# Kernel tuning notes

Measured on AMD Instinct MI355X. Metric: run time of the kernel, lower is better.

## Reference

```python
import jax, jax.numpy as jnp
import numpy as np

H = 8          # n_heads
LORA_SCALE = 1.0


def _lora(x, down, up):
    # nn.Linear convention: y = x @ W.T ; down:[r,in], up:[out,r]
    return (x @ down.T) @ up.T


def setup_inputs() -> dict:
    key = jax.random.key(0)
    ks = jax.random.split(key, 16)
    B, S, D, R = 4, 2048, 640, 4
    std = 1.0 / np.sqrt(D)
    inp = {
        "hidden_states": jax.random.normal(ks[0], (B, S, D), jnp.float32),
        "wq": jax.random.normal(ks[1], (D, D), jnp.float32) * std,
        "wk": jax.random.normal(ks[2], (D, D), jnp.float32) * std,
        "wv": jax.random.normal(ks[3], (D, D), jnp.float32) * std,
        "wo": jax.random.normal(ks[4], (D, D), jnp.float32) * std,
        "bo": jax.random.normal(ks[5], (D,), jnp.float32) * 0.02,
        "q_down": jax.random.normal(ks[6], (R, D), jnp.float32) * (1.0 / R),
        "q_up": jax.random.normal(ks[7], (D, R), jnp.float32) * 0.02,
        "k_down": jax.random.normal(ks[8], (R, D), jnp.float32) * (1.0 / R),
        "k_up": jax.random.normal(ks[9], (D, R), jnp.float32) * 0.02,
        "v_down": jax.random.normal(ks[10], (R, D), jnp.float32) * (1.0 / R),
        "v_up": jax.random.normal(ks[11], (D, R), jnp.float32) * 0.02,
        "o_down": jax.random.normal(ks[12], (R, D), jnp.float32) * (1.0 / R),
        "o_up": jax.random.normal(ks[13], (D, R), jnp.float32) * 0.02,
    }
    return inp


def reference(hidden_states, wq, wk, wv, wo, bo,
              q_down, q_up, k_down, k_up, v_down, v_up, o_down, o_up):
    B, S, D = hidden_states.shape
    hd = D // H
    sm_scale = 1.0 / np.sqrt(hd)

    x = hidden_states  # self-attention: encoder_hidden_states = hidden_states
    q = x @ wq.T + LORA_SCALE * _lora(x, q_down, q_up)
    k = x @ wk.T + LORA_SCALE * _lora(x, k_down, k_up)
    v = x @ wv.T + LORA_SCALE * _lora(x, v_down, v_up)

    # head_to_batch_dim: [B,S,D] -> [B,H,S,hd]
    q = q.reshape(B, S, H, hd).transpose(0, 2, 1, 3)
    k = k.reshape(B, S, H, hd).transpose(0, 2, 1, 3)
    v = v.reshape(B, S, H, hd).transpose(0, 2, 1, 3)

    # get_attention_scores: baddbmm(beta=0, alpha=1/sqrt(hd)) + softmax
    scores = jnp.einsum("bhqd,bhkd->bhqk", q, k) * sm_scale
    probs = jax.nn.softmax(scores, axis=-1)
    attn_out = jnp.einsum("bhqk,bhkd->bhqd", probs, v)

    # batch_to_head_dim: [B,H,S,hd] -> [B,S,D]
    attn_out = attn_out.transpose(0, 2, 1, 3).reshape(B, S, D)

    # out projection (with bias) + LoRA on the pre-projection hidden states
    out = attn_out @ wo.T + bo + LORA_SCALE * _lora(attn_out, o_down, o_up)
    # to_out[1] is dropout -> identity at eval
    return out
```

## Files before the change

### kernel.cpp

```cpp
#include <hip/hip_runtime.h>

typedef unsigned short u16;
typedef unsigned int u32;
typedef unsigned long long u64;

typedef __bf16 bf16x8 __attribute__((ext_vector_type(8)));
typedef float f32x4 __attribute__((ext_vector_type(4)));
typedef float f32x16 __attribute__((ext_vector_type(16)));

__device__ __forceinline__ float b2f(u16 u) {
    union { u32 i; float f; } c; c.i = ((u32)u) << 16; return c.f;
}
__device__ __forceinline__ u16 f2b(float f) {
    union { float f; u32 i; } c; c.f = f;
    u32 r = c.i + 0x7fffu + ((c.i >> 16) & 1u);
    return (u16)(r >> 16);
}
__device__ __forceinline__ u32 pack2(float a, float b) {
    return (u32)f2b(a) | ((u32)f2b(b) << 16);
}
__device__ __forceinline__ u32 cvt_pk_bf16(float a, float b) {
    u32 r;
    asm("v_cvt_pk_bf16_f32 %0, %1, %2" : "=v"(r) : "v"(a), "v"(b));
    return r;
}
__device__ __forceinline__ float fexp2(float x) {
    float r;
    asm("v_exp_f32 %0, %1" : "=v"(r) : "v"(x));
    return r;
}

__device__ __forceinline__ f32x4 mfma16(bf16x8 a, bf16x8 b, f32x4 c) {
    return __builtin_amdgcn_mfma_f32_16x16x32_bf16(a, b, c, 0, 0, 0);
}
__device__ __forceinline__ f32x16 mfma32(bf16x8 a, bf16x8 b, f32x16 c) {
    return __builtin_amdgcn_mfma_f32_32x32x16_bf16(a, b, c, 0, 0, 0);
}

__device__ __forceinline__ void lds_cp16(const u16* gsrc, u16* ldst) {
    __builtin_amdgcn_global_load_lds(
        (const __attribute__((address_space(1))) u32*)gsrc,
        (__attribute__((address_space(3))) u32*)ldst, 16, 0, 0);
}

struct ConvJobs {
    const float* s[4];
    const float* up[4];
    const float* dn[4];
    u16* d[4];
};

__global__ __launch_bounds__(256) void prep(ConvJobs J,
                                            const float* __restrict__ x,
                                            u16* __restrict__ xb,
                                            u16* __restrict__ vt, int do_pad) {
    int bx = blockIdx.x;
    if (bx < 1600) {
        int j = bx / 400;
        int i = (bx - j * 400) * 256 + threadIdx.x;
        int n = i / 160;
        int k4 = (i - n * 160) * 4;
        float4 w = ((const float4*)J.s[j])[i];
        float4 u = *(const float4*)(J.up[j] + n * 4);
        const float* dnp = J.dn[j];
        float4 d0 = *(const float4*)(dnp + k4);
        float4 d1 = *(const float4*)(dnp + 640 + k4);
        float4 d2 = *(const float4*)(dnp + 1280 + k4);
        float4 d3 = *(const float4*)(dnp + 1920 + k4);
        ushort4 o;
        o.x = f2b(w.x + u.x * d0.x + u.y * d1.x + u.z * d2.x + u.w * d3.x);
        o.y = f2b(w.y + u.x * d0.y + u.y * d1.y + u.z * d2.y + u.w * d3.y);
        o.z = f2b(w.z + u.x * d0.z + u.y * d1.z + u.z * d2.z + u.w * d3.z);
        o.w = f2b(w.w + u.x * d0.w + u.y * d1.w + u.z * d2.w + u.w * d3.w);
        ((ushort4*)J.d[j])[i] = o;
    } else if (bx < 2880) {
        int base = (bx - 1600) * 1024 + threadIdx.x;
#pragma unroll
        for (int it = 0; it < 4; ++it) {
            int i = base + it * 256;
            float4 v = ((const float4*)x)[i];
            ushort4 o;
            o.x = f2b(v.x); o.y = f2b(v.y); o.z = f2b(v.z); o.w = f2b(v.w);
            ((ushort4*)xb)[i] = o;
        }
    } else if (do_pad) {
        int idx = (bx - 2880) * 256 + threadIdx.x;
        int q = idx * 4;
        int bh = q >> 15;
        int rem = q & 32767;
        int row = rem >> 11, col = rem & 2047;
        u16 val = (row == 0) ? (u16)0x3F80 : (u16)0;
        ushort4 o = make_ushort4(val, val, val, val);
        *(ushort4*)(vt + ((size_t)bh * 96 + 80 + row) * 2048 + col) = o;
    }
}

struct QkvPtrs {
    const u16* W[3];
    void* out[3];
    float scale[3];
    int mode[3];
};

__global__ __launch_bounds__(256) void gemm_bt(const u16* __restrict__ A, QkvPtrs P,
                                               const float* __restrict__ bias) {
    int z = blockIdx.z;
    const u16* W = P.W[z];
    const float scl = P.scale[z];
    const int md = P.mode[z];
    int m0 = blockIdx.x * 128, n0 = blockIdx.y * 128;
    int tid = threadIdx.x, lane = tid & 63, wid = tid >> 6;
    int g = lane >> 4, l15 = lane & 15;
    __shared__ __align__(16) u16 smem[24576];
    u16* As_ = smem;
    u16* Bs_ = smem + 12288;
    f32x4 acc[4][4] = {};
    int wm = (wid & 1) * 64, wn = (wid >> 1) * 64;

    int r0 = tid >> 2, cb = (tid & 3) * 8;
    const u16* pA = A + (size_t)(m0 + r0) * 640 + cb;
    const u16* pB = W + (size_t)(n0 + r0) * 640 + cb;

    auto stage = [&](int buf, int k0) {
        u16* da = As_ + buf * 4096 + tid * 8;
        u16* db = Bs_ + buf * 4096 + tid * 8;
        lds_cp16(pA + k0, da);
        lds_cp16(pA + 40960 + k0, da + 2048);
        lds_cp16(pB + k0, db);
        lds_cp16(pB + 40960 + k0, db + 2048);
    };
    auto compute = [&](int cur) {
        const u16* as = As_ + cur * 4096;
        const u16* bs = Bs_ + cur * 4096;
        bf16x8 af[4], bfv[4];
#pragma unroll
        for (int q4 = 0; q4 < 4; ++q4) {
            af[q4]  = *(const bf16x8*)(as + (wm + q4 * 16 + l15) * 32 + g * 8);
            bfv[q4] = *(const bf16x8*)(bs + (wn + q4 * 16 + l15) * 32 + g * 8);
        }
#pragma unroll
        for (int i = 0; i < 4; ++i)
#pragma unroll
            for (int j = 0; j < 4; ++j)
                acc[i][j] = mfma16(af[i], bfv[j], acc[i][j]);
    };

    stage(0, 0);
    stage(1, 32);
    int cur = 0;
    for (int t = 0; t < 19; ++t) {
        asm volatile("s_waitcnt vmcnt(4)" ::: "memory");
        __builtin_amdgcn_s_barrier();
        asm volatile("" ::: "memory");
        if (t < 18) stage((cur == 0) ? 2 : cur - 1, (t + 2) * 32);
        compute(cur);
        cur = (cur == 2) ? 0 : cur + 1;
    }
    asm volatile("s_waitcnt vmcnt(0)" ::: "memory");
    __builtin_amdgcn_s_barrier();
    asm volatile("" ::: "memory");
    compute(cur);

    float bv[4];
#pragma unroll
    for (int j = 0; j < 4; ++j) {
        int n = n0 + wn + j * 16 + l15;
        bv[j] = (md == 1) ? bias[n] : 0.f;
    }

    if (md == 2) {
        __syncthreads();
        u16* Tl = smem;
#pragma unroll
        for (int i = 0; i < 4; ++i) {
#pragma unroll
            for (int j = 0; j < 4; ++j) {
                uint2 pk;
                pk.x = pack2(acc[i][j][0], acc[i][j][1]);
                pk.y = pack2(acc[i][j][2], acc[i][j][3]);
                *(uint2*)(Tl + (wn + j * 16 + l15) * 136 + wm + i * 16 + g * 4) = pk;
            }
        }
        __syncthreads();
        int bb2 = m0 >> 11;
        int sl0 = m0 & 2047;
        u16* outb_ = (u16*)P.out[z];
#pragma unroll
        for (int it = 0; it < 16; ++it) {
            int qq = it * 256 + tid;
            int row = qq >> 5;
            int pos = (qq & 31) * 4;
            int ss = (pos & ~12) | ((pos & 4) << 1) | ((pos & 8) >> 1);
            uint2 val = *(const uint2*)(Tl + row * 136 + ss);
            int n = n0 + row;
            int h = n / 80, d = n - h * 80;
            *(uint2*)(outb_ + (((size_t)bb2 * 8 + h) * 96 + d) * 2048 + sl0 + pos) = val;
        }
        return;
    }

    float* outf = (float*)P.out[z];
    u16* outb = (u16*)P.out[z];
#pragma unroll
    for (int i = 0; i < 4; ++i) {
#pragma unroll
        for (int r = 0; r < 4; ++r) {
            int m = m0 + wm + i * 16 + g * 4 + r;
#pragma unroll
            for (int j = 0; j < 4; ++j) {
                int n = n0 + wn + j * 16 + l15;
                float v = acc[i][j][r] + bv[j];
                if (md == 1) {
                    outf[(size_t)m * 640 + n] = v;
                } else {
                    int bb = m >> 11, s = m & 2047;
                    int h = n / 80, d = n - h * 80;
                    outb[(((size_t)bb * 8 + h) * 2048 + s) * 80 + d] = f2b(v * scl);
                }
            }
        }
    }
}

__global__ __launch_bounds__(256) void transpose_v(const u16* __restrict__ Vin,
                                                   u16* __restrict__ Vout) {
    __shared__ u32 lds32[64 * 41];
    int bh = blockIdx.y;
    int s0 = blockIdx.x * 64;
    int tid = threadIdx.x;
    const u16* in = Vin + (size_t)bh * 2048 * 80;
    u16* out = Vout + (size_t)bh * 96 * 2048;

    for (int t = tid; t < 640; t += 256) {
        int s = t / 10, c = t - s * 10;
        uint4 v = *(const uint4*)(in + (size_t)(s0 + s) * 80 + c * 8);
        u32* p = lds32 + s * 41 + c * 4;
        p[0] = v.x; p[1] = v.y; p[2] = v.z; p[3] = v.w;
    }
    __syncthreads();
    for (int t = tid; t < 640; t += 256) {
        int d = t >> 3, c8 = t & 7;
        int dp = d >> 1, hi = d & 1;
        u16 vals[8];
#pragma unroll
        for (int j = 0; j < 8; ++j) {
            u32 w = lds32[(c8 * 8 + j) * 41 + dp];
            vals[j] = hi ? (u16)(w >> 16) : (u16)(w & 0xffff);
        }
        u16* dst = out + (size_t)d * 2048 + s0 + (c8 >> 1) * 16 + (c8 & 1) * 4;
        *(uint2*)dst = *(const uint2*)(vals);
        *(uint2*)(dst + 8) = *(const uint2*)(vals + 4);
    }
    for (int t = tid; t < 1024; t += 256) {
        int r = t >> 6, c = t & 63;
        out[(size_t)(80 + r) * 2048 + s0 + c] = (r == 0) ? 0x3F80 : 0;
    }
}

__global__ __launch_bounds__(512) void flash_attn(const u16* __restrict__ Q,
                                                  const u16* __restrict__ K,
                                                  const u16* __restrict__ Vt_g,
                                                  u16* __restrict__ O) {
    int bh = blockIdx.y;
    int q0 = blockIdx.x * 256;
    int tid = threadIdx.x;
    int lane = tid & 63, wid = tid >> 6, l31 = lane & 31, h2 = lane >> 5;
    const size_t base = (size_t)bh * 2048 * 80;
    const size_t vbase = (size_t)bh * 96 * 2048;

    __shared__ __align__(16) u16 lds[2 * 5632 + 2 * 7200];
    u16* Ks0 = lds;
    u16* Vt0 = lds + 11264;

    bf16x8 qf[5];
    {
        int qrow = q0 + wid * 32 + l31;
#pragma unroll
        for (int ks = 0; ks < 5; ++ks)
            qf[ks] = *(const bf16x8*)(Q + base + (size_t)qrow * 80 + ks * 16 + h2 * 8);
    }

    f32x16 oa[3] = {};
    const float C2 = 17.312340490667562f;

    auto stage = [&](int buf, int kt) {
#pragma unroll
        for (int it = 0; it < 4; ++it) {
            int c = tid + it * 512;
            if (c < 704) {
                int row = c / 11, col = c - row * 11;
                lds_cp16(K + base + (size_t)(kt + row) * 80 + col * 8,
                         Ks0 + buf * 5632 + c * 8);
            } else if (c < 1600) {
                int t = c - 704;
                int row = t / 9, col = t - row * 9;
                lds_cp16(Vt_g + vbase + (size_t)row * 2048 + kt + col * 8,
                         Vt0 + buf * 7200 + t * 8);
            }
        }
    };

    stage(0, 0);
    __syncthreads();

    for (int i = 0; i < 32; ++i) {
        int cur = i & 1;
        if (i < 31) stage(cur ^ 1, (i + 1) * 64);

        const u16* ks = Ks0 + cur * 5632;
        const u16* vt = Vt0 + cur * 7200;

#pragma unroll
        for (int kk2 = 0; kk2 < 2; ++kk2) {
            f32x16 s = {};
            __builtin_amdgcn_s_setprio(1);
#pragma unroll
            for (int ks5 = 0; ks5 < 5; ++ks5) {
                bf16x8 kf = *(const bf16x8*)(ks + (kk2 * 32 + l31) * 88 + ks5 * 16 + h2 * 8);
                s = mfma32(kf, qf[ks5], s);
            }
            __builtin_amdgcn_s_setprio(0);
            u32 d[8];
#pragma unroll
            for (int j = 0; j < 8; ++j)
                d[j] = cvt_pk_bf16(fexp2(s[2 * j] - C2), fexp2(s[2 * j + 1] - C2));
            __builtin_amdgcn_s_setprio(1);
#pragma unroll
            for (int sl = 0; sl < 2; ++sl) {
                union { u32 w[4]; bf16x8 v; } pa;
                pa.w[0] = d[4 * sl + 0];
                pa.w[1] = d[4 * sl + 1];
                pa.w[2] = d[4 * sl + 2];
                pa.w[3] = d[4 * sl + 3];
#pragma unroll
                for (int nt = 0; nt < 3; ++nt) {
                    bf16x8 vf = *(const bf16x8*)(vt + (nt * 32 + l31) * 72 +
                                                 kk2 * 32 + sl * 16 + h2 * 8);
                    oa[nt] = mfma32(pa.v, vf, oa[nt]);
                }
            }
            __builtin_amdgcn_s_setprio(0);
        }
        __syncthreads();
    }

    int b = bh >> 3, h = bh & 7;
    float inv[16];
#pragma unroll
    for (int reg = 0; reg < 16; ++reg)
        inv[reg] = 1.f / __shfl(oa[2][reg], (lane & 32) + 16, 64);
#pragma unroll
    for (int nt = 0; nt < 3; ++nt) {
        int vd = nt * 32 + l31;
        if (vd < 80) {
#pragma unroll
            for (int reg = 0; reg < 16; ++reg) {
                int q = q0 + wid * 32 + (reg & 3) + 8 * (reg >> 2) + 4 * h2;
                O[((size_t)(b * 2048 + q)) * 640 + h * 80 + vd] = f2b(oa[nt][reg] * inv[reg]);
            }
        }
    }
}

extern "C" void kernel_launch(void* const* d_in, const int* in_sizes, int n_in,
                              void* d_out, int out_size, void* d_ws, size_t ws_size,
                              hipStream_t stream) {
    const float* x      = (const float*)d_in[0];
    const float* wq     = (const float*)d_in[1];
    const float* wk     = (const float*)d_in[2];
    const float* wv     = (const float*)d_in[3];
    const float* wo     = (const float*)d_in[4];
    const float* bo     = (const float*)d_in[5];
    const float* q_down = (const float*)d_in[6];
    const float* q_up   = (const float*)d_in[7];
    const float* k_down = (const float*)d_in[8];
    const float* k_up   = (const float*)d_in[9];
    const float* v_down = (const float*)d_in[10];
    const float* v_up   = (const float*)d_in[11];
    const float* o_down = (const float*)d_in[12];
    const float* o_up   = (const float*)d_in[13];

    char* ws = (char*)d_ws;
    u16* xb    = (u16*)(ws);
    u16* wbv   = (u16*)(ws + 10485760);
    u16* wbq   = (u16*)(ws + 11304960);
    u16* wbk   = (u16*)(ws + 12124160);
    u16* wbo   = (u16*)(ws + 12943360);
    u16* q_ws  = (u16*)(ws + 13762560);
    u16* k_ws  = (u16*)(ws + 24248320);
    u16* v_ws  = (u16*)(ws + 34734080);
    u16* attn  = (u16*)(ws + 45219840);

    const size_t vt_off = 56360960;
    const size_t vt_need = vt_off + 12582912 + 16384;
    const bool direct_vt = (ws_size >= vt_need);
    u16* vT_ws = direct_vt ? (u16*)(ws + vt_off)
                           : (u16*)(ws);

    ConvJobs cj;
    cj.s[0] = wq; cj.up[0] = q_up; cj.dn[0] = q_down; cj.d[0] = wbq;
    cj.s[1] = wk; cj.up[1] = k_up; cj.dn[1] = k_down; cj.d[1] = wbk;
    cj.s[2] = wv; cj.up[2] = v_up; cj.dn[2] = v_down; cj.d[2] = wbv;
    cj.s[3] = wo; cj.up[3] = o_up; cj.dn[3] = o_down; cj.d[3] = wbo;
    prep<<<3904, 256, 0, stream>>>(cj, x, xb, vT_ws, direct_vt ? 1 : 0);

    QkvPtrs pq;
    pq.W[0] = wbq; pq.W[1] = wbk; pq.W[2] = wbv;
    pq.out[0] = q_ws; pq.out[1] = k_ws;
    pq.out[2] = direct_vt ? (void*)vT_ws : (void*)v_ws;
    pq.scale[0] = 0.11180339887498949f * 1.4426950408889634f;
    pq.scale[1] = 1.0f;
    pq.scale[2] = 1.0f;
    pq.mode[0] = 0; pq.mode[1] = 0; pq.mode[2] = direct_vt ? 2 : 0;
    gemm_bt<<<dim3(64, 5, 3), 256, 0, stream>>>(xb, pq, bo);

    if (!direct_vt)
        transpose_v<<<dim3(32, 32), 256, 0, stream>>>(v_ws, vT_ws);

    flash_attn<<<dim3(8, 32), 512, 0, stream>>>(q_ws, k_ws, vT_ws, attn);

    QkvPtrs po;
    po.W[0] = wbo; po.W[1] = wbo; po.W[2] = wbo;
    po.out[0] = d_out; po.out[1] = d_out; po.out[2] = d_out;
    po.scale[0] = 1.0f; po.scale[1] = 1.0f; po.scale[2] = 1.0f;
    po.mode[0] = 1; po.mode[1] = 1; po.mode[2] = 1;
    gemm_bt<<<dim3(64, 5, 1), 256, 0, stream>>>(attn, po, bo);
}
```

Measured before the change: 193.8 us.

## Fuse prep, QKV GEMM, flash attention and out-proj into one persistent kernel

Replaces the chain of separate launches (weight/activation prep, QKV GEMM, flash attention, output projection) with a single 256-block persistent kernel whose phases are separated by atomic-counter grid barriers. The GEMM phases are rewritten for 512-thread blocks with a different per-wave tile, and the flash attention body is factored into a shared device function. The aim is to remove launch overhead and inter-kernel gaps. In exchange, GEMM tiles now run on a fixed 256-block grid with several tiles per block, and the spin barriers assume all 256 blocks are co-resident, which risks deadlock if they are not.

```diff
diff --git a/kernel.cpp b/kernel.cpp
--- a/kernel.cpp
+++ b/kernel.cpp
@@ -50,10 +50,323 @@
     u16* d[4];
 };
 
-__global__ __launch_bounds__(256) void prep(ConvJobs J,
-                                            const float* __restrict__ x,
-                                            u16* __restrict__ xb,
-                                            u16* __restrict__ vt, int do_pad) {
+__device__ __forceinline__ void gridbar(u32* cnt, int idx) {
+    __syncthreads();
+    __threadfence();
+    if (threadIdx.x == 0) {
+        atomicAdd(&cnt[idx], 1u);
+        while (atomicAdd(&cnt[idx], 0u) < 256u) __builtin_amdgcn_s_sleep(2);
+    }
+    __syncthreads();
+    __threadfence();
+}
+
+__device__ __forceinline__ void gemm_tile512(const u16* __restrict__ Ap,
+                                             const u16* __restrict__ W,
+                                             void* outp, float scl, int md,
+                                             const float* __restrict__ bias,
+                                             int m0, int n0, u16* smem) {
+    int tid = threadIdx.x, lane = tid & 63, wid = tid >> 6;
+    int g = lane >> 4, l15 = lane & 15;
+    u16* As_ = smem;
+    u16* Bs_ = smem + 12288;
+    f32x4 acc[4][2] = {};
+    int wm = (wid & 1) * 64, wn = (wid >> 1) * 32;
+
+    int r0 = tid >> 2, cb = (tid & 3) * 8;
+    const u16* pA = Ap + (size_t)(m0 + r0) * 640 + cb;
+    const u16* pB = W + (size_t)(n0 + r0) * 640 + cb;
+
+    __syncthreads();
+
+    auto stage = [&](int buf, int k0) {
+        lds_cp16(pA + k0, As_ + buf * 4096 + tid * 8);
+        lds_cp16(pB + k0, Bs_ + buf * 4096 + tid * 8);
+    };
+    auto compute = [&](int cur) {
+        const u16* as = As_ + cur * 4096;
+        const u16* bs = Bs_ + cur * 4096;
+        bf16x8 af[4], bfv[2];
+#pragma unroll
+        for (int i = 0; i < 4; ++i)
+            af[i] = *(const bf16x8*)(as + (wm + i * 16 + l15) * 32 + g * 8);
+#pragma unroll
+        for (int j = 0; j < 2; ++j)
+            bfv[j] = *(const bf16x8*)(bs + (wn + j * 16 + l15) * 32 + g * 8);
+#pragma unroll
+        for (int i = 0; i < 4; ++i)
+#pragma unroll
+            for (int j = 0; j < 2; ++j)
+                acc[i][j] = mfma16(af[i], bfv[j], acc[i][j]);
+    };
+
+    stage(0, 0);
+    stage(1, 32);
+    int cur = 0;
+    for (int t = 0; t < 19; ++t) {
+        asm volatile("s_waitcnt vmcnt(2)" ::: "memory");
+        __builtin_amdgcn_s_barrier();
+        asm volatile("" ::: "memory");
+        if (t < 18) stage((cur == 0) ? 2 : cur - 1, (t + 2) * 32);
+        compute(cur);
+        cur = (cur == 2) ? 0 : cur + 1;
+    }
+    asm volatile("s_waitcnt vmcnt(0)" ::: "memory");
+    __builtin_amdgcn_s_barrier();
+    asm volatile("" ::: "memory");
+    compute(cur);
+
+    if (md == 2) {
+        __syncthreads();
+        u16* Tl = smem;
+#pragma unroll
+        for (int i = 0; i < 4; ++i) {
+#pragma unroll
+            for (int j = 0; j < 2; ++j) {
+                uint2 pk;
+                pk.x = pack2(acc[i][j][0], acc[i][j][1]);
+                pk.y = pack2(acc[i][j][2], acc[i][j][3]);
+                *(uint2*)(Tl + (wn + j * 16 + l15) * 136 + wm + i * 16 + g * 4) = pk;
+            }
+        }
+        __syncthreads();
+        int bb2 = m0 >> 11;
+        int sl0 = m0 & 2047;
+        u16* outb_ = (u16*)outp;
+#pragma unroll
+        for (int it = 0; it < 8; ++it) {
+            int qq = it * 512 + tid;
+            int row = qq >> 5;
+            int pos = (qq & 31) * 4;
+            int ss = (pos & ~12) | ((pos & 4) << 1) | ((pos & 8) >> 1);
+            uint2 val = *(const uint2*)(Tl + row * 136 + ss);
+            int n = n0 + row;
+            int h = n / 80, d = n - h * 80;
+            *(uint2*)(outb_ + (((size_t)bb2 * 8 + h) * 96 + d) * 2048 + sl0 + pos) = val;
+        }
+        __syncthreads();
+        return;
+    }
+
+    float bv[2];
+#pragma unroll
+    for (int j = 0; j < 2; ++j)
+        bv[j] = (md == 1) ? bias[n0 + wn + j * 16 + l15] : 0.f;
+    float* outf = (float*)outp;
+    u16* outb = (u16*)outp;
+#pragma unroll
+    for (int i = 0; i < 4; ++i) {
+#pragma unroll
+        for (int r = 0; r < 4; ++r) {
+            int m = m0 + wm + i * 16 + g * 4 + r;
+#pragma unroll
+            for (int j = 0; j < 2; ++j) {
+                int n = n0 + wn + j * 16 + l15;
+                float v = acc[i][j][r] + bv[j];
+                if (md == 1) {
+                    outf[(size_t)m * 640 + n] = v;
+                } else {
+                    int bb = m >> 11, s = m & 2047;
+                    int h = n / 80, d = n - h * 80;
+                    outb[(((size_t)bb * 8 + h) * 2048 + s) * 80 + d] = f2b(v * scl);
+                }
+            }
+        }
+    }
+}
+
+__device__ __forceinline__ void flash512(int bid, const u16* __restrict__ Q,
+                                         const u16* __restrict__ K,
+                                         const u16* __restrict__ Vt_g,
+                                         u16* __restrict__ O, u16* lds) {
+    int q0 = (bid & 7) * 256;
+    int bh = bid >> 3;
+    int tid = threadIdx.x;
+    int lane = tid & 63, wid = tid >> 6, l31 = lane & 31, h2 = lane >> 5;
+    const size_t base = (size_t)bh * 2048 * 80;
+    const size_t vbase = (size_t)bh * 96 * 2048;
+
+    u16* Ks0 = lds;
+    u16* Vt0 = lds + 11264;
+
+    bf16x8 qf[5];
+    {
+        int qrow = q0 + wid * 32 + l31;
+#pragma unroll
+        for (int ks = 0; ks < 5; ++ks)
+            qf[ks] = *(const bf16x8*)(Q + base + (size_t)qrow * 80 + ks * 16 + h2 * 8);
+    }
+
+    f32x16 oa[3] = {};
+    const float C2 = 17.312340490667562f;
+
+    auto stage = [&](int buf, int kt) {
+#pragma unroll
+        for (int it = 0; it < 4; ++it) {
+            int c = tid + it * 512;
+            if (c < 704) {
+                int row = c / 11, col = c - row * 11;
+                lds_cp16(K + base + (size_t)(kt + row) * 80 + col * 8,
+                         Ks0 + buf * 5632 + c * 8);
+            } else if (c < 1600) {
+                int t = c - 704;
+                int row = t / 9, col = t - row * 9;
+                lds_cp16(Vt_g + vbase + (size_t)row * 2048 + kt + col * 8,
+                         Vt0 + buf * 7200 + t * 8);
+            }
+        }
+    };
+
+    stage(0, 0);
+    __syncthreads();
+
+    for (int i = 0; i < 32; ++i) {
+        int cur = i & 1;
+        if (i < 31) stage(cur ^ 1, (i + 1) * 64);
+
+        const u16* ks = Ks0 + cur * 5632;
+        const u16* vt = Vt0 + cur * 7200;
+
+#pragma unroll
+        for (int kk2 = 0; kk2 < 2; ++kk2) {
+            f32x16 s = {};
+            __builtin_amdgcn_s_setprio(1);
+#pragma unroll
+            for (int ks5 = 0; ks5 < 5; ++ks5) {
+                bf16x8 kf = *(const bf16x8*)(ks + (kk2 * 32 + l31) * 88 + ks5 * 16 + h2 * 8);
+                s = mfma32(kf, qf[ks5], s);
+            }
+            __builtin_amdgcn_s_setprio(0);
+            u32 d[8];
+#pragma unroll
+            for (int j = 0; j < 8; ++j)
+                d[j] = cvt_pk_bf16(fexp2(s[2 * j] - C2), fexp2(s[2 * j + 1] - C2));
+            __builtin_amdgcn_s_setprio(1);
+#pragma unroll
+            for (int sl = 0; sl < 2; ++sl) {
+                union { u32 w[4]; bf16x8 v; } pa;
+                pa.w[0] = d[4 * sl + 0];
+                pa.w[1] = d[4 * sl + 1];
+                pa.w[2] = d[4 * sl + 2];
+                pa.w[3] = d[4 * sl + 3];
+#pragma unroll
+                for (int nt = 0; nt < 3; ++nt) {
+                    bf16x8 vf = *(const bf16x8*)(vt + (nt * 32 + l31) * 72 +
+                                                 kk2 * 32 + sl * 16 + h2 * 8);
+                    oa[nt] = mfma32(pa.v, vf, oa[nt]);
+                }
+            }
+            __builtin_amdgcn_s_setprio(0);
+        }
+        __syncthreads();
+    }
+
+    int b = bh >> 3, h = bh & 7;
+    float inv[16];
+#pragma unroll
+    for (int reg = 0; reg < 16; ++reg)
+        inv[reg] = 1.f / __shfl(oa[2][reg], (lane & 32) + 16, 64);
+#pragma unroll
+    for (int nt = 0; nt < 3; ++nt) {
+        int vd = nt * 32 + l31;
+        if (vd < 80) {
+#pragma unroll
+            for (int reg = 0; reg < 16; ++reg) {
+                int q = q0 + wid * 32 + (reg & 3) + 8 * (reg >> 2) + 4 * h2;
+                O[((size_t)(b * 2048 + q)) * 640 + h * 80 + vd] = f2b(oa[nt][reg] * inv[reg]);
+            }
+        }
+    }
+}
+
+struct FusedArgs {
+    ConvJobs cj;
+    const float* x;
+    u16* xb;
+    u16* vt;
+    u16* q_ws;
+    u16* k_ws;
+    u16* attn;
+    const float* bias;
+    float* out;
+    u32* cnt;
+};
+
+__global__ __launch_bounds__(512) void fused(FusedArgs A) {
+    __shared__ __align__(16) u16 smem[25856];
+    int bid = blockIdx.x, tid = threadIdx.x;
+
+    {
+        const int WE = 409600;
+        const int XE = WE + 1310720;
+        const int PE = XE + 262144;
+        for (int u = bid * 512 + tid; u < PE; u += 131072) {
+            if (u < WE) {
+                int j = u / 102400;
+                int i = u - j * 102400;
+                int n = i / 160;
+                int k4 = (i - n * 160) * 4;
+                float4 w = ((const float4*)A.cj.s[j])[i];
+                float4 uu = *(const float4*)(A.cj.up[j] + n * 4);
+                const float* dnp = A.cj.dn[j];
+                float4 d0 = *(const float4*)(dnp + k4);
+                float4 d1 = *(const float4*)(dnp + 640 + k4);
+                float4 d2 = *(const float4*)(dnp + 1280 + k4);
+                float4 d3 = *(const float4*)(dnp + 1920 + k4);
+                ushort4 o;
+                o.x = f2b(w.x + uu.x * d0.x + uu.y * d1.x + uu.z * d2.x + uu.w * d3.x);
+                o.y = f2b(w.y + uu.x * d0.y + uu.y * d1.y + uu.z * d2.y + uu.w * d3.y);
+                o.z = f2b(w.z + uu.x * d0.z + uu.y * d1.z + uu.z * d2.z + uu.w * d3.z);
+                o.w = f2b(w.w + uu.x * d0.w + uu.y * d1.w + uu.z * d2.w + uu.w * d3.w);
+                ((ushort4*)A.cj.d[j])[i] = o;
+            } else if (u < XE) {
+                int i = u - WE;
+                float4 v = ((const float4*)A.x)[i];
+                ushort4 o;
+                o.x = f2b(v.x); o.y = f2b(v.y); o.z = f2b(v.z); o.w = f2b(v.w);
+                ((ushort4*)A.xb)[i] = o;
+            } else {
+                int idx = u - XE;
+                int q = idx * 4;
+                int bh = q >> 15;
+                int rem = q & 32767;
+                int row = rem >> 11, col = rem & 2047;
+                u16 val = (row == 0) ? (u16)0x3F80 : (u16)0;
+                ushort4 o = make_ushort4(val, val, val, val);
+                *(ushort4*)(A.vt + ((size_t)bh * 96 + 80 + row) * 2048 + col) = o;
+            }
+        }
+    }
+    gridbar(A.cnt, 0);
+
+    const float qscale = 0.11180339887498949f * 1.4426950408889634f;
+    for (int t = bid; t < 960; t += 256) {
+        int xm = t & 63;
+        int r = t >> 6;
+        int yn = r % 5, z = r / 5;
+        const u16* Wz = (z == 0) ? (const u16*)A.cj.d[0]
+                      : (z == 1) ? (const u16*)A.cj.d[1] : (const u16*)A.cj.d[2];
+        void* oz = (z == 0) ? (void*)A.q_ws : (z == 1) ? (void*)A.k_ws : (void*)A.vt;
+        float sz = (z == 0) ? qscale : 1.f;
+        int mz = (z == 2) ? 2 : 0;
+        gemm_tile512(A.xb, Wz, oz, sz, mz, A.bias, xm * 128, yn * 128, smem);
+    }
+    gridbar(A.cnt, 1);
+
+    flash512(bid, A.q_ws, A.k_ws, A.vt, A.attn, smem);
+    gridbar(A.cnt, 2);
+
+    for (int t = bid; t < 320; t += 256) {
+        int xm = t & 63, yn = t >> 6;
+        gemm_tile512(A.attn, (const u16*)A.cj.d[3], A.out, 1.f, 1, A.bias,
+                     xm * 128, yn * 128, smem);
+    }
+}
+
+__global__ __launch_bounds__(256) void prep4(ConvJobs J,
+                                             const float* __restrict__ x,
+                                             u16* __restrict__ xb,
+                                             u16* __restrict__ vt, int do_pad) {
     int bx = blockIdx.x;
     if (bx < 1600) {
         int j = bx / 400;
@@ -163,10 +476,8 @@
 
     float bv[4];
 #pragma unroll
-    for (int j = 0; j < 4; ++j) {
-        int n = n0 + wn + j * 16 + l15;
-        bv[j] = (md == 1) ? bias[n] : 0.f;
-    }
+    for (int j = 0; j < 4; ++j)
+        bv[j] = (md == 1) ? bias[n0 + wn + j * 16 + l15] : 0.f;
 
     if (md == 2) {
         __syncthreads();
@@ -261,105 +572,9 @@
                                                   const u16* __restrict__ K,
                                                   const u16* __restrict__ Vt_g,
                                                   u16* __restrict__ O) {
-    int bh = blockIdx.y;
-    int q0 = blockIdx.x * 256;
-    int tid = threadIdx.x;
-    int lane = tid & 63, wid = tid >> 6, l31 = lane & 31, h2 = lane >> 5;
-    const size_t base = (size_t)bh * 2048 * 80;
-    const size_t vbase = (size_t)bh * 96 * 2048;
-
     __shared__ __align__(16) u16 lds[2 * 5632 + 2 * 7200];
-    u16* Ks0 = lds;
-    u16* Vt0 = lds + 11264;
-
-    bf16x8 qf[5];
-    {
-        int qrow = q0 + wid * 32 + l31;
-#pragma unroll
-        for (int ks = 0; ks < 5; ++ks)
-            qf[ks] = *(const bf16x8*)(Q + base + (size_t)qrow * 80 + ks * 16 + h2 * 8);
-    }
-
-    f32x16 oa[3] = {};
-    const float C2 = 17.312340490667562f;
-
-    auto stage = [&](int buf, int kt) {
-#pragma unroll
-        for (int it = 0; it < 4; ++it) {
-            int c = tid + it * 512;
-            if (c < 704) {
-                int row = c / 11, col = c - row * 11;
-                lds_cp16(K + base + (size_t)(kt + row) * 80 + col * 8,
-                         Ks0 + buf * 5632 + c * 8);
-            } else if (c < 1600) {
-                int t = c - 704;
-                int row = t / 9, col = t - row * 9;
-                lds_cp16(Vt_g + vbase + (size_t)row * 2048 + kt + col * 8,
-                         Vt0 + buf * 7200 + t * 8);
-            }
-        }
-    };
-
-    stage(0, 0);
-    __syncthreads();
-
-    for (int i = 0; i < 32; ++i) {
-        int cur = i & 1;
-        if (i < 31) stage(cur ^ 1, (i + 1) * 64);
-
-        const u16* ks = Ks0 + cur * 5632;
-        const u16* vt = Vt0 + cur * 7200;
-
-#pragma unroll
-        for (int kk2 = 0; kk2 < 2; ++kk2) {
-            f32x16 s = {};
-            __builtin_amdgcn_s_setprio(1);
-#pragma unroll
-            for (int ks5 = 0; ks5 < 5; ++ks5) {
-                bf16x8 kf = *(const bf16x8*)(ks + (kk2 * 32 + l31) * 88 + ks5 * 16 + h2 * 8);
-                s = mfma32(kf, qf[ks5], s);
-            }
-            __builtin_amdgcn_s_setprio(0);
-            u32 d[8];
-#pragma unroll
-            for (int j = 0; j < 8; ++j)
-                d[j] = cvt_pk_bf16(fexp2(s[2 * j] - C2), fexp2(s[2 * j + 1] - C2));
-            __builtin_amdgcn_s_setprio(1);
-#pragma unroll
-            for (int sl = 0; sl < 2; ++sl) {
-                union { u32 w[4]; bf16x8 v; } pa;
-                pa.w[0] = d[4 * sl + 0];
-                pa.w[1] = d[4 * sl + 1];
-                pa.w[2] = d[4 * sl + 2];
-                pa.w[3] = d[4 * sl + 3];
-#pragma unroll
-                for (int nt = 0; nt < 3; ++nt) {
-                    bf16x8 vf = *(const bf16x8*)(vt + (nt * 32 + l31) * 72 +
-                                                 kk2 * 32 + sl * 16 + h2 * 8);
-                    oa[nt] = mfma32(pa.v, vf, oa[nt]);
-                }
-            }
-            __builtin_amdgcn_s_setprio(0);
-        }
-        __syncthreads();
-    }
-
-    int b = bh >> 3, h = bh & 7;
-    float inv[16];
-#pragma unroll
-    for (int reg = 0; reg < 16; ++reg)
-        inv[reg] = 1.f / __shfl(oa[2][reg], (lane & 32) + 16, 64);
-#pragma unroll
-    for (int nt = 0; nt < 3; ++nt) {
-        int vd = nt * 32 + l31;
-        if (vd < 80) {
-#pragma unroll
-            for (int reg = 0; reg < 16; ++reg) {
-                int q = q0 + wid * 32 + (reg & 3) + 8 * (reg >> 2) + 4 * h2;
-                O[((size_t)(b * 2048 + q)) * 640 + h * 80 + vd] = f2b(oa[nt][reg] * inv[reg]);
-            }
-        }
-    }
+    int bid = blockIdx.x + blockIdx.y * 8;
+    flash512(((bid & 255) & 7) | ((bid >> 3) << 3) ? bid : bid, Q, K, Vt_g, O, lds);
 }
 
 extern "C" void kernel_launch(void* const* d_in, const int* in_sizes, int n_in,
@@ -392,17 +607,31 @@
     u16* attn  = (u16*)(ws + 45219840);
 
     const size_t vt_off = 56360960;
-    const size_t vt_need = vt_off + 12582912 + 16384;
-    const bool direct_vt = (ws_size >= vt_need);
-    u16* vT_ws = direct_vt ? (u16*)(ws + vt_off)
-                           : (u16*)(ws);
+    const size_t vt_end = vt_off + 12582912 + 16384;
+    const size_t cnt_off = vt_end;
+    const bool fused_ok = (ws_size >= cnt_off + 64);
+    const bool direct_vt = (ws_size >= vt_end);
+    u16* vT_ws = direct_vt ? (u16*)(ws + vt_off) : (u16*)(ws);
 
     ConvJobs cj;
     cj.s[0] = wq; cj.up[0] = q_up; cj.dn[0] = q_down; cj.d[0] = wbq;
     cj.s[1] = wk; cj.up[1] = k_up; cj.dn[1] = k_down; cj.d[1] = wbk;
     cj.s[2] = wv; cj.up[2] = v_up; cj.dn[2] = v_down; cj.d[2] = wbv;
     cj.s[3] = wo; cj.up[3] = o_up; cj.dn[3] = o_down; cj.d[3] = wbo;
-    prep<<<3904, 256, 0, stream>>>(cj, x, xb, vT_ws, direct_vt ? 1 : 0);
+
+    if (fused_ok) {
+        u32* cnt = (u32*)(ws + cnt_off);
+        hipMemsetAsync(cnt, 0, 64, stream);
+        FusedArgs fa;
+        fa.cj = cj;
+        fa.x = x; fa.xb = xb; fa.vt = vT_ws;
+        fa.q_ws = q_ws; fa.k_ws = k_ws; fa.attn = attn;
+        fa.bias = bo; fa.out = (float*)d_out; fa.cnt = cnt;
+        fused<<<256, 512, 0, stream>>>(fa);
+        return;
+    }
+
+    prep4<<<3904, 256, 0, stream>>>(cj, x, xb, vT_ws, direct_vt ? 1 : 0);
 
     QkvPtrs pq;
     pq.W[0] = wbq; pq.W[1] = wbk; pq.W[2] = wbv;
```

New measurement: 446.6 us. +130.4%, slower.
